# Performance work log

Hardware: AMD Instinct MI355X
Metric: run time of the kernel (lower is better)

Reference implementation:

```python
import jax, jax.numpy as jnp
import numpy as np

B, T = 256, 2048
VOCAB, EMB, HID, OUT = 7, 20, 128, 6


def setup_inputs() -> dict:
    key = jax.random.key(0)
    ks = jax.random.split(key, 9)
    s_ih = 1.0 / np.sqrt(HID)
    inp = {
        "inputs": jax.random.randint(ks[0], (B, T), 0, VOCAB),
        "c0": jax.random.normal(ks[1], (1, B, HID), dtype=jnp.float32),
        # PyTorch LSTM params (gate order i,f,g,o), uniform(-1/sqrt(H), 1/sqrt(H))
        "W_ih": jax.random.uniform(ks[2], (4 * HID, EMB), jnp.float32, -s_ih, s_ih),
        "W_hh": jax.random.uniform(ks[3], (4 * HID, HID), jnp.float32, -s_ih, s_ih),
        "b_ih": jax.random.uniform(ks[4], (4 * HID,), jnp.float32, -s_ih, s_ih),
        "b_hh": jax.random.uniform(ks[5], (4 * HID,), jnp.float32, -s_ih, s_ih),
        "W_fc": jax.random.uniform(ks[6], (OUT, HID), jnp.float32, -s_ih, s_ih),
        "b_fc": jax.random.uniform(ks[7], (OUT,), jnp.float32, -s_ih, s_ih),
        "emb": jax.random.normal(ks[8], (VOCAB, EMB), dtype=jnp.float32),
    }
    return inp


def _lstm(x_gates, h0, c0, W_hh):
    # x_gates: [T, B, 4H] precomputed input contributions (+ both biases)
    def step(carry, xg):
        h, c = carry
        gates = xg + h @ W_hh.T  # [B, 4H]
        i, f, g, o = jnp.split(gates, 4, axis=-1)
        i, f, o = jax.nn.sigmoid(i), jax.nn.sigmoid(f), jax.nn.sigmoid(o)
        g = jnp.tanh(g)
        c = f * c + i * g
        h = o * jnp.tanh(c)
        return (h, c), h

    (_, _), hs = jax.lax.scan(step, (h0, c0), x_gates)
    return hs  # [T, B, H]


def reference(inputs, c0, W_ih, W_hh, b_ih, b_hh, W_fc, b_fc, emb):
    x = emb[inputs]  # [B, T, EMB]
    # precompute input-to-gate projection once (batched GEMM)
    x_gates = jnp.einsum("bte,ge->btg", x, W_ih) + (b_ih + b_hh)  # [B,T,4H]
    x_gates = jnp.transpose(x_gates, (1, 0, 2))  # [T, B, 4H]
    h0 = jnp.zeros((B, HID), dtype=x.dtype)
    hs = _lstm(x_gates, h0, c0[0], W_hh)  # [T, B, H]
    hiddens = jnp.transpose(hs, (1, 0, 2))  # [B, T, H]
    logits = jnp.einsum("bth,oh->bto", hiddens, W_fc) + b_fc
    return jax.nn.softmax(logits, axis=2)
```

## Files before the change

### kernel.cpp

```cpp
#include <hip/hip_runtime.h>
#include <math.h>

#define BB 256
#define TT 2048
#define VOCAB 7
#define EMBD 20
#define HID 128
#define OUTD 6
#define CHUNK 64
#define NCHUNK (TT / CHUNK)

typedef _Float16 h2 __attribute__((ext_vector_type(2)));

__device__ __forceinline__ float v_exp2(float x) {
    float r; asm("v_exp_f32 %0, %1" : "=v"(r) : "v"(x)); return r;
}
__device__ __forceinline__ float v_rcp(float x) {
    float r; asm("v_rcp_f32 %0, %1" : "=v"(r) : "v"(x)); return r;
}
__device__ __forceinline__ float sigmoid_f(float x) {
    return v_rcp(1.0f + v_exp2(-1.44269504f * x));
}
__device__ __forceinline__ float tanh_f(float x) {
    float ax = fabsf(x);
    float t = v_exp2(-2.88539008f * ax);
    float r = (1.0f - t) * v_rcp(1.0f + t);
    return __builtin_copysignf(r, x);
}

#if defined(__has_builtin)
#if __has_builtin(__builtin_amdgcn_fdot2)
#define HAS_FDOT2 1
#endif
#endif

__device__ __forceinline__ float dot2acc(h2 a, h2 b, float c) {
#ifdef HAS_FDOT2
    return __builtin_amdgcn_fdot2(a, b, c, false);
#else
    return c + (float)a.x * (float)b.x + (float)a.y * (float)b.y;
#endif
}

#define KEEP(x) asm volatile("" : "+v"(x))

__global__ __launch_bounds__(512, 2) void lstm_persist(
    const int* __restrict__ inputs, const float* __restrict__ c0,
    const float* __restrict__ W_ih, const float* __restrict__ W_hh,
    const float* __restrict__ b_ih, const float* __restrict__ b_hh,
    const float* __restrict__ W_fc, const float* __restrict__ b_fc,
    const float* __restrict__ emb, float* __restrict__ out)
{
    __shared__ float gtab[VOCAB][4 * HID];
    __shared__ h2    hbuf[CHUNK][HID / 2];
    __shared__ int   toks[CHUNK];

    const int tid  = threadIdx.x;
    const int b    = blockIdx.x;
    const int j    = tid >> 2;
    const int r    = tid & 3;
    const int lane = tid & 63;
    const int wave = tid >> 6;

    h2 w[HID / 2];
    {
        const float2* wr = (const float2*)(W_hh + (size_t)(r * HID + j) * HID);
        #pragma unroll
        for (int k = 0; k < HID / 2; ++k) {
            float2 f = wr[k];
            h2 p; p.x = (_Float16)f.x; p.y = (_Float16)f.y;
            w[k] = p;
        }
    }
    #pragma unroll
    for (int k = 0; k < HID / 2; ++k) KEEP(w[k]);

    {
        const int g = r * HID + j;
        float wih[EMBD];
        #pragma unroll
        for (int e = 0; e < EMBD; ++e) wih[e] = W_ih[g * EMBD + e];
        float bb = b_ih[g] + b_hh[g];
        #pragma unroll
        for (int v = 0; v < VOCAB; ++v) {
            float a = bb;
            #pragma unroll
            for (int e = 0; e < EMBD; ++e) a += wih[e] * emb[v * EMBD + e];
            gtab[v][tid] = a;
        }
    }

    float c = c0[b * HID + j];
    if (tid < HID / 2) {
        h2 z; z.x = (_Float16)0.f; z.y = (_Float16)0.f;
        hbuf[CHUNK - 1][tid] = z;
    }
    __syncthreads();

    #pragma unroll 1
    for (int ch = 0; ch < NCHUNK; ++ch) {
        const int t0 = ch * CHUNK;
        if (tid < CHUNK) toks[tid] = inputs[(size_t)b * TT + t0 + tid];
        __syncthreads();

        #pragma unroll 1
        for (int s = 0; s < CHUNK; ++s) {
            const int prev = (s + CHUNK - 1) & (CHUNK - 1);
            const float xg = gtab[toks[s]][tid];

            const uint4* hp = (const uint4*)&hbuf[prev][0];
            float a0 = 0.f, a1 = 0.f, a2 = 0.f, a3 = 0.f;
            #pragma unroll
            for (int k = 0; k < 16; ++k) {
                uint4 v = hp[k];
                a0 = dot2acc(w[4 * k + 0], __builtin_bit_cast(h2, v.x), a0);
                a1 = dot2acc(w[4 * k + 1], __builtin_bit_cast(h2, v.y), a1);
                a2 = dot2acc(w[4 * k + 2], __builtin_bit_cast(h2, v.z), a2);
                a3 = dot2acc(w[4 * k + 3], __builtin_bit_cast(h2, v.w), a3);
            }
            float pre = (a0 + a1) + (a2 + a3) + xg;

            float act = (r == 2) ? tanh_f(pre) : sigmoid_f(pre);

            float x1 = __shfl_xor(act, 1, 64);
            float x2 = __shfl_xor(act, 2, 64);
            float x3 = __shfl_xor(act, 3, 64);
            const bool b1 = (r & 1), b2 = (r & 2) != 0;
            float gi = b2 ? (b1 ? x3 : x2) : (b1 ? x1 : act);
            float gf = b2 ? (b1 ? x2 : x3) : (b1 ? act : x1);
            float gg = b2 ? (b1 ? x1 : act) : (b1 ? x3 : x2);
            float go = b2 ? (b1 ? act : x1) : (b1 ? x2 : x3);

            c = gf * c + gi * gg;
            float h = go * tanh_f(c);
            if (r == 0) ((_Float16*)&hbuf[s][0])[j] = (_Float16)h;
            __syncthreads();
        }

        {
            float wfc0[OUTD], wfc1[OUTD];
            #pragma unroll
            for (int o = 0; o < OUTD; ++o) {
                wfc0[o] = W_fc[o * HID + 2 * lane];
                wfc1[o] = W_fc[o * HID + 2 * lane + 1];
            }
            #pragma unroll 1
            for (int i = 0; i < CHUNK / 8; ++i) {
                const int row = wave * (CHUNK / 8) + i;
                h2 hv = hbuf[row][lane];
                float h0 = (float)hv.x, h1 = (float)hv.y;
                float acc[OUTD];
                #pragma unroll
                for (int o = 0; o < OUTD; ++o) acc[o] = wfc0[o] * h0 + wfc1[o] * h1;
                #pragma unroll
                for (int off = 32; off >= 1; off >>= 1) {
                    #pragma unroll
                    for (int o = 0; o < OUTD; ++o) acc[o] += __shfl_xor(acc[o], off, 64);
                }
                if (lane == 0) {
                    float m = -1e30f;
                    #pragma unroll
                    for (int o = 0; o < OUTD; ++o) { acc[o] += b_fc[o]; m = fmaxf(m, acc[o]); }
                    float e[OUTD], ssum = 0.f;
                    #pragma unroll
                    for (int o = 0; o < OUTD; ++o) { e[o] = v_exp2(1.44269504f * (acc[o] - m)); ssum += e[o]; }
                    float inv = v_rcp(ssum);
                    float* po = out + ((size_t)b * TT + (t0 + row)) * OUTD;
                    #pragma unroll
                    for (int o = 0; o < OUTD; ++o) po[o] = e[o] * inv;
                }
            }
        }
        __syncthreads();
    }
}

extern "C" void kernel_launch(void* const* d_in, const int* in_sizes, int n_in,
                              void* d_out, int out_size, void* d_ws, size_t ws_size,
                              hipStream_t stream) {
    const int*   inputs = (const int*)  d_in[0];
    const float* c0     = (const float*)d_in[1];
    const float* W_ih   = (const float*)d_in[2];
    const float* W_hh   = (const float*)d_in[3];
    const float* b_ih   = (const float*)d_in[4];
    const float* b_hh   = (const float*)d_in[5];
    const float* W_fc   = (const float*)d_in[6];
    const float* b_fc   = (const float*)d_in[7];
    const float* emb    = (const float*)d_in[8];
    float* out = (float*)d_out;

    lstm_persist<<<BB, 512, 0, stream>>>(inputs, c0, W_ih, W_hh, b_ih, b_hh,
                                         W_fc, b_fc, emb, out);
}
```

Before: 1.606 ms.

## Split hidden-dim K across lanes, compute all four gates per thread, pad LDS for one block/CU

Changes the work split so each of the four threads per hidden unit handles a quarter of the K dimension for all four gates. Partial sums are then reduced with xor shuffles, replacing the old scheme where each thread owned one gate and exchanged activations. The gate table is stored as float4 so one read returns all four gate inputs. A 96KB unused shared-memory pad (written behind a never-true guard) forces one block per CU, and launch bounds drop the minimum of 2 blocks. Also switches to inline v_dot2 asm and hoists the FC weight loads out of the chunk loop. Each thread now evaluates all five transcendentals, which is redundant across the four lanes, and running one block per CU may reduce latency hiding.

```diff
diff --git a/kernel.cpp b/kernel.cpp
--- a/kernel.cpp
+++ b/kernel.cpp
@@ -28,32 +28,25 @@
     return __builtin_copysignf(r, x);
 }
 
-#if defined(__has_builtin)
-#if __has_builtin(__builtin_amdgcn_fdot2)
-#define HAS_FDOT2 1
-#endif
-#endif
-
-__device__ __forceinline__ float dot2acc(h2 a, h2 b, float c) {
-#ifdef HAS_FDOT2
-    return __builtin_amdgcn_fdot2(a, b, c, false);
-#else
-    return c + (float)a.x * (float)b.x + (float)a.y * (float)b.y;
-#endif
+__device__ __forceinline__ float dot2(h2 a, h2 b, float c) {
+    float d;
+    asm("v_dot2_f32_f16 %0, %1, %2, %3" : "=v"(d) : "v"(a), "v"(b), "v"(c));
+    return d;
 }
 
 #define KEEP(x) asm volatile("" : "+v"(x))
 
-__global__ __launch_bounds__(512, 2) void lstm_persist(
+__global__ __launch_bounds__(512) void lstm_persist(
     const int* __restrict__ inputs, const float* __restrict__ c0,
     const float* __restrict__ W_ih, const float* __restrict__ W_hh,
     const float* __restrict__ b_ih, const float* __restrict__ b_hh,
     const float* __restrict__ W_fc, const float* __restrict__ b_fc,
     const float* __restrict__ emb, float* __restrict__ out)
 {
-    __shared__ float gtab[VOCAB][4 * HID];
-    __shared__ h2    hbuf[CHUNK][HID / 2];
-    __shared__ int   toks[CHUNK];
+    __shared__ float4   gtab[VOCAB][HID];
+    __shared__ _Float16 hbuf[CHUNK][HID];
+    __shared__ int      toks[CHUNK];
+    __shared__ char     ldspad[96 * 1024];
 
     const int tid  = threadIdx.x;
     const int b    = blockIdx.x;
@@ -62,18 +55,25 @@
     const int lane = tid & 63;
     const int wave = tid >> 6;
 
-    h2 w[HID / 2];
+    if (__builtin_expect(inputs[0] == -2147483647, 0)) ldspad[tid] = 1;
+
+    h2 w0[16], w1[16], w2[16], w3[16];
     {
-        const float2* wr = (const float2*)(W_hh + (size_t)(r * HID + j) * HID);
+        const float2* p0 = (const float2*)(W_hh + ((size_t)(0 * HID + j) * HID + r * 32));
+        const float2* p1 = (const float2*)(W_hh + ((size_t)(1 * HID + j) * HID + r * 32));
+        const float2* p2 = (const float2*)(W_hh + ((size_t)(2 * HID + j) * HID + r * 32));
+        const float2* p3 = (const float2*)(W_hh + ((size_t)(3 * HID + j) * HID + r * 32));
         #pragma unroll
-        for (int k = 0; k < HID / 2; ++k) {
-            float2 f = wr[k];
-            h2 p; p.x = (_Float16)f.x; p.y = (_Float16)f.y;
-            w[k] = p;
+        for (int k = 0; k < 16; ++k) {
+            float2 f0 = p0[k], f1 = p1[k], f2 = p2[k], f3 = p3[k];
+            h2 a; a.x = (_Float16)f0.x; a.y = (_Float16)f0.y; w0[k] = a;
+            h2 bq; bq.x = (_Float16)f1.x; bq.y = (_Float16)f1.y; w1[k] = bq;
+            h2 cq; cq.x = (_Float16)f2.x; cq.y = (_Float16)f2.y; w2[k] = cq;
+            h2 dq; dq.x = (_Float16)f3.x; dq.y = (_Float16)f3.y; w3[k] = dq;
         }
     }
     #pragma unroll
-    for (int k = 0; k < HID / 2; ++k) KEEP(w[k]);
+    for (int k = 0; k < 16; ++k) { KEEP(w0[k]); KEEP(w1[k]); KEEP(w2[k]); KEEP(w3[k]); }
 
     {
         const int g = r * HID + j;
@@ -86,14 +86,19 @@
             float a = bb;
             #pragma unroll
             for (int e = 0; e < EMBD; ++e) a += wih[e] * emb[v * EMBD + e];
-            gtab[v][tid] = a;
+            ((float*)&gtab[v][j])[r] = a;
         }
     }
 
     float c = c0[b * HID + j];
-    if (tid < HID / 2) {
-        h2 z; z.x = (_Float16)0.f; z.y = (_Float16)0.f;
-        hbuf[CHUNK - 1][tid] = z;
+    if (tid < HID) hbuf[CHUNK - 1][tid] = (_Float16)0.f;
+
+    float wfc0[OUTD], wfc1[OUTD], bfc[OUTD];
+    #pragma unroll
+    for (int o = 0; o < OUTD; ++o) {
+        wfc0[o] = W_fc[o * HID + 2 * lane];
+        wfc1[o] = W_fc[o * HID + 2 * lane + 1];
+        bfc[o]  = b_fc[o];
     }
     __syncthreads();
 
@@ -106,69 +111,65 @@
         #pragma unroll 1
         for (int s = 0; s < CHUNK; ++s) {
             const int prev = (s + CHUNK - 1) & (CHUNK - 1);
-            const float xg = gtab[toks[s]][tid];
 
-            const uint4* hp = (const uint4*)&hbuf[prev][0];
+            const uint4* hp = (const uint4*)&hbuf[prev][r * 32];
             float a0 = 0.f, a1 = 0.f, a2 = 0.f, a3 = 0.f;
             #pragma unroll
-            for (int k = 0; k < 16; ++k) {
+            for (int k = 0; k < 4; ++k) {
                 uint4 v = hp[k];
-                a0 = dot2acc(w[4 * k + 0], __builtin_bit_cast(h2, v.x), a0);
-                a1 = dot2acc(w[4 * k + 1], __builtin_bit_cast(h2, v.y), a1);
-                a2 = dot2acc(w[4 * k + 2], __builtin_bit_cast(h2, v.z), a2);
-                a3 = dot2acc(w[4 * k + 3], __builtin_bit_cast(h2, v.w), a3);
+                h2 hx = __builtin_bit_cast(h2, v.x);
+                h2 hy = __builtin_bit_cast(h2, v.y);
+                h2 hz = __builtin_bit_cast(h2, v.z);
+                h2 hw = __builtin_bit_cast(h2, v.w);
+                a0 = dot2(w0[4*k+0], hx, a0); a0 = dot2(w0[4*k+1], hy, a0);
+                a0 = dot2(w0[4*k+2], hz, a0); a0 = dot2(w0[4*k+3], hw, a0);
+                a1 = dot2(w1[4*k+0], hx, a1); a1 = dot2(w1[4*k+1], hy, a1);
+                a1 = dot2(w1[4*k+2], hz, a1); a1 = dot2(w1[4*k+3], hw, a1);
+                a2 = dot2(w2[4*k+0], hx, a2); a2 = dot2(w2[4*k+1], hy, a2);
+                a2 = dot2(w2[4*k+2], hz, a2); a2 = dot2(w2[4*k+3], hw, a2);
+                a3 = dot2(w3[4*k+0], hx, a3); a3 = dot2(w3[4*k+1], hy, a3);
+                a3 = dot2(w3[4*k+2], hz, a3); a3 = dot2(w3[4*k+3], hw, a3);
             }
-            float pre = (a0 + a1) + (a2 + a3) + xg;
+            a0 += __shfl_xor(a0, 1, 64); a0 += __shfl_xor(a0, 2, 64);
+            a1 += __shfl_xor(a1, 1, 64); a1 += __shfl_xor(a1, 2, 64);
+            a2 += __shfl_xor(a2, 1, 64); a2 += __shfl_xor(a2, 2, 64);
+            a3 += __shfl_xor(a3, 1, 64); a3 += __shfl_xor(a3, 2, 64);
 
-            float act = (r == 2) ? tanh_f(pre) : sigmoid_f(pre);
-
-            float x1 = __shfl_xor(act, 1, 64);
-            float x2 = __shfl_xor(act, 2, 64);
-            float x3 = __shfl_xor(act, 3, 64);
-            const bool b1 = (r & 1), b2 = (r & 2) != 0;
-            float gi = b2 ? (b1 ? x3 : x2) : (b1 ? x1 : act);
-            float gf = b2 ? (b1 ? x2 : x3) : (b1 ? act : x1);
-            float gg = b2 ? (b1 ? x1 : act) : (b1 ? x3 : x2);
-            float go = b2 ? (b1 ? act : x1) : (b1 ? x2 : x3);
-
+            const float4 xg = gtab[toks[s]][j];
+            float gi = sigmoid_f(a0 + xg.x);
+            float gf = sigmoid_f(a1 + xg.y);
+            float gg = tanh_f  (a2 + xg.z);
+            float go = sigmoid_f(a3 + xg.w);
             c = gf * c + gi * gg;
             float h = go * tanh_f(c);
-            if (r == 0) ((_Float16*)&hbuf[s][0])[j] = (_Float16)h;
+            if (r == 0) hbuf[s][j] = (_Float16)h;
             __syncthreads();
         }
 
-        {
-            float wfc0[OUTD], wfc1[OUTD];
+        #pragma unroll 1
+        for (int i = 0; i < CHUNK / 8; ++i) {
+            const int row = wave * (CHUNK / 8) + i;
+            h2 hv = ((const h2*)&hbuf[row][0])[lane];
+            float h0 = (float)hv.x, h1 = (float)hv.y;
+            float acc[OUTD];
             #pragma unroll
-            for (int o = 0; o < OUTD; ++o) {
-                wfc0[o] = W_fc[o * HID + 2 * lane];
-                wfc1[o] = W_fc[o * HID + 2 * lane + 1];
+            for (int o = 0; o < OUTD; ++o) acc[o] = wfc0[o] * h0 + wfc1[o] * h1;
+            #pragma unroll
+            for (int off = 32; off >= 1; off >>= 1) {
+                #pragma unroll
+                for (int o = 0; o < OUTD; ++o) acc[o] += __shfl_xor(acc[o], off, 64);
             }
-            #pragma unroll 1
-            for (int i = 0; i < CHUNK / 8; ++i) {
-                const int row = wave * (CHUNK / 8) + i;
-                h2 hv = hbuf[row][lane];
-                float h0 = (float)hv.x, h1 = (float)hv.y;
-                float acc[OUTD];
+            if (lane == 0) {
+                float m = -1e30f;
                 #pragma unroll
-                for (int o = 0; o < OUTD; ++o) acc[o] = wfc0[o] * h0 + wfc1[o] * h1;
+                for (int o = 0; o < OUTD; ++o) { acc[o] += bfc[o]; m = fmaxf(m, acc[o]); }
+                float e[OUTD], ssum = 0.f;
                 #pragma unroll
-                for (int off = 32; off >= 1; off >>= 1) {
-                    #pragma unroll
-                    for (int o = 0; o < OUTD; ++o) acc[o] += __shfl_xor(acc[o], off, 64);
-                }
-                if (lane == 0) {
-                    float m = -1e30f;
-                    #pragma unroll
-                    for (int o = 0; o < OUTD; ++o) { acc[o] += b_fc[o]; m = fmaxf(m, acc[o]); }
-                    float e[OUTD], ssum = 0.f;
-                    #pragma unroll
-                    for (int o = 0; o < OUTD; ++o) { e[o] = v_exp2(1.44269504f * (acc[o] - m)); ssum += e[o]; }
-                    float inv = v_rcp(ssum);
-                    float* po = out + ((size_t)b * TT + (t0 + row)) * OUTD;
-                    #pragma unroll
-                    for (int o = 0; o < OUTD; ++o) po[o] = e[o] * inv;
-                }
+                for (int o = 0; o < OUTD; ++o) { e[o] = v_exp2(1.44269504f * (acc[o] - m)); ssum += e[o]; }
+                float inv = v_rcp(ssum);
+                float* po = out + ((size_t)b * TT + (t0 + row)) * OUTD;
+                #pragma unroll
+                for (int o = 0; o < OUTD; ++o) po[o] = e[o] * inv;
             }
         }
         __syncthreads();
```

After: 1.570 ms. 2.2% less time.
